# Kernel tuning notes

Hardware: AMD Instinct MI355X
Metric: run time of the kernel (lower is better)

## Reference

```python
import jax, jax.numpy as jnp
import numpy as np

BS, P, D = 64, 300, 1024
NUM_CLASSES = 150


def setup_inputs() -> dict:
    key = jax.random.key(0)
    ks = jax.random.split(key, 12)
    s = 0.02
    return {
        "x": jax.random.normal(ks[0], (BS * P, D), jnp.float32),
        "subject": jax.random.normal(ks[1], (BS, D), jnp.float32),
        "obj": jax.random.normal(ks[2], (BS, D), jnp.float32),
        "relation": jax.random.normal(ks[3], (BS, D), jnp.float32),
        "W_theta": jax.random.normal(ks[4], (D, D), jnp.float32) * s,
        "b_theta": jax.random.normal(ks[5], (D,), jnp.float32) * s,
        "W_pair": jax.random.normal(ks[6], (3 * D, 1), jnp.float32) * s,
        "b_pair": jax.random.normal(ks[7], (1,), jnp.float32) * s,
        "W_cls": jax.random.normal(ks[8], (2 * D, 1), jnp.float32) * s,
        "b_cls": jax.random.normal(ks[9], (1,), jnp.float32) * s,
        "W_bbox": jax.random.normal(ks[10], (D, (NUM_CLASSES + 1) * 4), jnp.float32) * s,
        "b_bbox": jax.random.normal(ks[11], ((NUM_CLASSES + 1) * 4,), jnp.float32) * s,
    }


def reference(x, subject, obj, relation, W_theta, b_theta, W_pair, b_pair,
              W_cls, b_cls, W_bbox, b_bbox):
    bs = relation.shape[0]
    rel = relation @ W_theta + b_theta  # (bs, D)
    xb = x.reshape(bs, P, D)

    # cls_score_pair(concat([x1, x2, rel])) decomposed into 3 sliced matmuls.
    # x1[b,i,j] = x[b,j] (cols), x2[b,i,j] = x[b,i] (rows).
    Wa, Wb, Wc = W_pair[:D, 0], W_pair[D:2 * D, 0], W_pair[2 * D:, 0]
    col_term = xb @ Wa          # (bs, P) -> broadcast over rows i
    row_term = xb @ Wb          # (bs, P) -> broadcast over cols j
    rel_term = rel @ Wc + b_pair[0]  # (bs,)
    pair_score = jax.nn.sigmoid(row_term[:, :, None] + col_term[None if False else slice(None), None, :]
                                + rel_term[:, None, None])  # (bs, P, P)

    # cls_score on [x, subject] and [x, object]
    W1, W2 = W_cls[:D, 0], W_cls[D:, 0]
    xw = xb @ W1                                  # (bs, P)
    s_score = jax.nn.sigmoid(xw + (subject @ W2 + b_cls[0])[:, None])  # (bs, P)
    o_score = jax.nn.sigmoid(xw + (obj @ W2 + b_cls[0])[:, None])      # (bs, P)

    pair_score = pair_score * o_score[:, None, :] * s_score[:, :, None]

    x_subj = jnp.stack([1.0 - s_score, s_score], axis=-1).reshape(-1, 2)
    x_obj = jnp.stack([1.0 - o_score, o_score], axis=-1).reshape(-1, 2)

    bbox_deltas = x @ W_bbox + b_bbox  # (bs*P, (C+1)*4)
    return (x_subj, x_obj, pair_score, bbox_deltas)
```

## Files before the change

### kernel.cpp

```cpp
#include <hip/hip_runtime.h>

#define PP    300
#define DD    1024
#define NOUT  604
#define NROWS 19200
#define OFF_PAIR  76800
#define OFF_BBOX  5836800

typedef unsigned short u16;
typedef __attribute__((ext_vector_type(8))) short bf16x8;
typedef __attribute__((ext_vector_type(4))) float f32x4;

#define GLOBAL_AS __attribute__((address_space(1)))
#define LDS_AS    __attribute__((address_space(3)))

__device__ inline u16 f2bf(float f) {
    unsigned u = __float_as_uint(f);
    return (u16)((u + 0x7fffu + ((u >> 16) & 1u)) >> 16);
}
__device__ inline float dot4(float4 a, float4 b) {
    return fmaf(a.x, b.x, fmaf(a.y, b.y, fmaf(a.z, b.z, a.w * b.w)));
}
__device__ inline float sigmoidf(float z) { return 1.f / (1.f + __expf(-z)); }

__global__ __launch_bounds__(256) void k_rows_raw(
        const float* __restrict__ x, const float* __restrict__ Wpair,
        const float* __restrict__ Wcls,
        float* __restrict__ colv, float* __restrict__ rowp,
        float* __restrict__ cwv, u16* __restrict__ xb,
        const float* __restrict__ Wbbox, u16* __restrict__ Bt,
        const float* __restrict__ Wt, float* __restrict__ v) {
    __shared__ float tile[32][33];
    if (blockIdx.x >= 5440) {
        int wave = threadIdx.x >> 6, lane = threadIdx.x & 63;
        int k = (blockIdx.x - 5440) * 4 + wave;
        const float4* row = (const float4*)(Wt + (size_t)k * DD);
        const float4* wc  = (const float4*)(Wpair + 2 * DD);
        float s = 0.f;
#pragma unroll
        for (int i = 0; i < 4; ++i) s += dot4(row[i * 64 + lane], wc[i * 64 + lane]);
#pragma unroll
        for (int off = 32; off; off >>= 1) s += __shfl_down(s, off, 64);
        if (lane == 0) v[k] = s;
        return;
    }
    if (blockIdx.x >= 4800) {
        int blk = blockIdx.x - 4800;
        int tid = threadIdx.x;
        int k0 = (blk & 31) * 32;
        int n0 = (blk >> 5) * 32;
        int tx = tid & 31;
        int ty = tid >> 5;
#pragma unroll
        for (int i = 0; i < 4; ++i) {
            int k = k0 + ty + i * 8;
            int n = n0 + tx;
            tile[ty + i * 8][tx] = (n < NOUT) ? Wbbox[(size_t)k * NOUT + n] : 0.f;
        }
        __syncthreads();
#pragma unroll
        for (int i = 0; i < 4; ++i) {
            int n = n0 + ty + i * 8;
            int k = k0 + tx;
            Bt[(size_t)n * DD + k] = f2bf(tile[tx][ty + i * 8]);
        }
        return;
    }
    int wave = threadIdx.x >> 6, lane = threadIdx.x & 63;
    int r = blockIdx.x * 4 + wave;
    const float4* xr = (const float4*)(x + (size_t)r * DD);
    const float4* wa = (const float4*)(Wpair);
    const float4* wb = (const float4*)(Wpair + DD);
    const float4* w1 = (const float4*)(Wcls);
    float ca = 0.f, cb = 0.f, cw = 0.f;
#pragma unroll
    for (int i = 0; i < 4; ++i) {
        int idx = i * 64 + lane;
        float4 xv = xr[idx];
        ca += dot4(xv, wa[idx]);
        cb += dot4(xv, wb[idx]);
        cw += dot4(xv, w1[idx]);
        unsigned lo = __builtin_amdgcn_perm(__float_as_uint(xv.y), __float_as_uint(xv.x), 0x07060302u);
        unsigned hi = __builtin_amdgcn_perm(__float_as_uint(xv.w), __float_as_uint(xv.z), 0x07060302u);
        *(uint2*)(xb + (size_t)r * DD + idx * 4) = make_uint2(lo, hi);
    }
#pragma unroll
    for (int off = 32; off; off >>= 1) {
        ca += __shfl_down(ca, off, 64);
        cb += __shfl_down(cb, off, 64);
        cw += __shfl_down(cw, off, 64);
    }
    if (lane == 0) {
        colv[r] = ca;
        rowp[r] = cb;
        cwv[r]  = cw;
    }
}

__global__ void k_scalars(const float* __restrict__ relation, const float* __restrict__ subject,
                          const float* __restrict__ obj, const float* __restrict__ btheta,
                          const float* __restrict__ Wpair, const float* __restrict__ bpair,
                          const float* __restrict__ Wcls, const float* __restrict__ bcls,
                          const float* __restrict__ v,
                          float* __restrict__ relt, float* __restrict__ subc,
                          float* __restrict__ objc) {
    __shared__ float red[4];
    int wave = threadIdx.x >> 6, lane = threadIdx.x & 63;
    int b = blockIdx.x;
    const float4* aa;
    const float4* bb;
    if (wave == 0)      { aa = (const float4*)(relation + (size_t)b * DD); bb = (const float4*)v; }
    else if (wave == 1) { aa = (const float4*)(subject + (size_t)b * DD);  bb = (const float4*)(Wcls + DD); }
    else if (wave == 2) { aa = (const float4*)(obj + (size_t)b * DD);      bb = (const float4*)(Wcls + DD); }
    else                { aa = (const float4*)btheta;                      bb = (const float4*)(Wpair + 2 * DD); }
    float s = 0.f;
#pragma unroll
    for (int i = 0; i < 4; ++i) s += dot4(aa[i * 64 + lane], bb[i * 64 + lane]);
#pragma unroll
    for (int off = 32; off; off >>= 1) s += __shfl_down(s, off, 64);
    if (lane == 0) red[wave] = s;
    __syncthreads();
    if (threadIdx.x == 0) {
        relt[b] = red[0] + red[3] + bpair[0];
        subc[b] = red[1] + bcls[0];
        objc[b] = red[2] + bcls[0];
    }
}

#define BKK 64
#define NSTEP 16

#define WAITCNT_VM(N) asm volatile("s_waitcnt vmcnt(" #N ")" ::: "memory")

#define STAGE_TILE(buf, k0)                                                                  \
    _Pragma("unroll")                                                                        \
    for (int q = 0; q < 4; ++q) {                                                            \
        int rowblk = q * 32 + wave * 8;                                                      \
        const u16* ga = a_base + (size_t)(rowblk + s_row) * DD + (k0) + s_c16 * 8;           \
        __builtin_amdgcn_global_load_lds((const GLOBAL_AS unsigned int*)ga,                  \
                                         (LDS_AS unsigned int*)(As[buf] + rowblk * BKK),     \
                                         16, 0, 0);                                          \
        const u16* gb = b_base + (size_t)(rowblk + s_row) * DD + (k0) + s_c16 * 8;           \
        __builtin_amdgcn_global_load_lds((const GLOBAL_AS unsigned int*)gb,                  \
                                         (LDS_AS unsigned int*)(Bs[buf] + rowblk * BKK),     \
                                         16, 0, 0);                                          \
    }

#define COMPUTE_TILE(buf)                                                                    \
    _Pragma("unroll")                                                                        \
    for (int kk = 0; kk < BKK; kk += 32) {                                                   \
        bf16x8 af[4], bfv[4];                                                                \
        int cx = (((kk >> 3) + quad) ^ (l16 & 7)) * 8;                                       \
        _Pragma("unroll")                                                                    \
        for (int f = 0; f < 4; ++f) {                                                        \
            int m = wr * 64 + f * 16 + l16;                                                  \
            af[f] = *(const bf16x8*)(As[buf] + m * BKK + cx);                                \
            int n = wc * 64 + f * 16 + l16;                                                  \
            bfv[f] = *(const bf16x8*)(Bs[buf] + n * BKK + cx);                               \
        }                                                                                    \
        _Pragma("unroll")                                                                    \
        for (int fi = 0; fi < 4; ++fi)                                                       \
            _Pragma("unroll")                                                                \
            for (int fj = 0; fj < 4; ++fj)                                                   \
                acc[fi][fj] = __builtin_amdgcn_mfma_f32_16x16x32_bf16(                       \
                    af[fi], bfv[fj], acc[fi][fj], 0, 0, 0);                                  \
    }

__global__ __launch_bounds__(256) void k_fused(
        const u16* __restrict__ xb, const u16* __restrict__ bt,
        const float* __restrict__ bias, float* __restrict__ outb,
        const float* __restrict__ rowp, const float* __restrict__ colv,
        const float* __restrict__ cwv,
        const float* __restrict__ relt, const float* __restrict__ subc,
        const float* __restrict__ objc,
        float* __restrict__ outx, float* __restrict__ pout) {
    __shared__ u16 As[2][128 * BKK] __attribute__((aligned(16)));
    __shared__ u16 Bs[2][128 * BKK] __attribute__((aligned(16)));

    int gbid = blockIdx.x;
    if (gbid < 760) {
        int xcd = gbid & 7;
        int rest = gbid >> 3;
        int n_t = rest % 5;
        int m_t = (rest / 5) * 8 + xcd;
        if (m_t >= 150) return;

        int tid = threadIdx.x;
        int wave = tid >> 6;
        int lane = tid & 63;
        int wr = wave >> 1, wc = wave & 1;
        int quad = lane >> 4;
        int l16 = lane & 15;

        f32x4 acc[4][4] = {};

        const u16* a_base = xb + (size_t)m_t * 128 * DD;
        const u16* b_base = bt + (size_t)n_t * 128 * DD;
        int s_row = lane >> 3;
        int s_c16 = (lane & 7) ^ s_row;

        STAGE_TILE(0, 0)

#pragma unroll 1
        for (int t = 0; t < NSTEP; t += 2) {
            STAGE_TILE(1, (t + 1) * BKK)
            WAITCNT_VM(8);
            __builtin_amdgcn_s_barrier();
            COMPUTE_TILE(0)
            __builtin_amdgcn_s_barrier();
            if (t + 2 < NSTEP) {
                STAGE_TILE(0, (t + 2) * BKK)
                WAITCNT_VM(8);
            } else {
                WAITCNT_VM(0);
            }
            __builtin_amdgcn_s_barrier();
            COMPUTE_TILE(1)
            __builtin_amdgcn_s_barrier();
        }

#pragma unroll
        for (int fj = 0; fj < 4; ++fj) {
            int col = n_t * 128 + wc * 64 + fj * 16 + l16;
            if (col < NOUT) {
                float bia = bias[col];
#pragma unroll
                for (int fi = 0; fi < 4; ++fi) {
#pragma unroll
                    for (int rg = 0; rg < 4; ++rg) {
                        int row = m_t * 128 + wr * 64 + fi * 16 + quad * 4 + rg;
                        outb[(size_t)row * NOUT + col] = acc[fi][fj][rg] + bia;
                    }
                }
            }
        }
    } else {
        float* cb_s = (float*)As;
        float* ob_s = ((float*)As) + 300;
        float* cw_s = ((float*)As) + 600;
        int blk = gbid - 760;
        int b = blk / 30;
        int chunk = blk - b * 30;
        int r0 = b * 300 + chunk * 10;
        int tid = threadIdx.x;
        float relt_b = relt[b], subc_b = subc[b], objc_b = objc[b];
        for (int j = tid; j < 300; j += 256) {
            cb_s[j] = colv[b * 300 + j];
            float cwj = cwv[b * 300 + j];
            cw_s[j] = cwj;
            ob_s[j] = sigmoidf(cwj + objc_b);
        }
        __syncthreads();
        if (tid < 150) {
            float c0 = cb_s[2 * tid], c1 = cb_s[2 * tid + 1];
            float o0 = ob_s[2 * tid], o1 = ob_s[2 * tid + 1];
#pragma unroll
            for (int rr = 0; rr < 10; ++rr) {
                int r = r0 + rr;
                int lr = chunk * 10 + rr;
                float rp = rowp[r] + relt_b;
                float ss = sigmoidf(cw_s[lr] + subc_b);
                float p0 = sigmoidf(rp + c0) * o0 * ss;
                float p1 = sigmoidf(rp + c1) * o1 * ss;
                ((float2*)(pout + (size_t)r * 300))[tid] = make_float2(p0, p1);
            }
        } else if (tid < 160) {
            int rr = tid - 150;
            int r = r0 + rr;
            int lr = chunk * 10 + rr;
            float sv = sigmoidf(cw_s[lr] + subc_b);
            float ov = sigmoidf(cw_s[lr] + objc_b);
            ((float2*)outx)[r]         = make_float2(1.f - sv, sv);
            ((float2*)outx)[NROWS + r] = make_float2(1.f - ov, ov);
        }
    }
}

__global__ __launch_bounds__(256) void k_prep(const float* __restrict__ Wbbox, u16* __restrict__ Bt,
                                              const float* __restrict__ Wt, const float* __restrict__ Wpair,
                                              float* __restrict__ v) {
    __shared__ float tile[32][33];
    int blk = blockIdx.x;
    int tid = threadIdx.x;
    if (blk < 640) {
        int k0 = (blk & 31) * 32;
        int n0 = (blk >> 5) * 32;
        int tx = tid & 31;
        int ty = tid >> 5;
#pragma unroll
        for (int i = 0; i < 4; ++i) {
            int k = k0 + ty + i * 8;
            int n = n0 + tx;
            tile[ty + i * 8][tx] = (n < NOUT) ? Wbbox[(size_t)k * NOUT + n] : 0.f;
        }
        __syncthreads();
#pragma unroll
        for (int i = 0; i < 4; ++i) {
            int n = n0 + ty + i * 8;
            int k = k0 + tx;
            Bt[(size_t)n * DD + k] = f2bf(tile[tx][ty + i * 8]);
        }
    } else {
        int wave = tid >> 6, lane = tid & 63;
        int k = (blk - 640) * 4 + wave;
        const float4* row = (const float4*)(Wt + (size_t)k * DD);
        const float4* wc  = (const float4*)(Wpair + 2 * DD);
        float s = 0.f;
#pragma unroll
        for (int i = 0; i < 4; ++i) s += dot4(row[i * 64 + lane], wc[i * 64 + lane]);
#pragma unroll
        for (int off = 32; off; off >>= 1) s += __shfl_down(s, off, 64);
        if (lane == 0) v[k] = s;
    }
}

__global__ __launch_bounds__(256) void k_rows_sa(
        const float* __restrict__ x, const float* __restrict__ Wpair,
        const float* __restrict__ Wcls,
        const float* __restrict__ relt, const float* __restrict__ subc,
        const float* __restrict__ objc,
        float* __restrict__ colv, float* __restrict__ rowp,
        float* __restrict__ sarr, float* __restrict__ oarr,
        float* __restrict__ out) {
    int wave = threadIdx.x >> 6, lane = threadIdx.x & 63;
    int r = blockIdx.x * 4 + wave;
    const float4* xr = (const float4*)(x + (size_t)r * DD);
    const float4* wa = (const float4*)(Wpair);
    const float4* wb = (const float4*)(Wpair + DD);
    const float4* w1 = (const float4*)(Wcls);
    float ca = 0.f, cb = 0.f, cw = 0.f;
#pragma unroll
    for (int i = 0; i < 4; ++i) {
        int idx = i * 64 + lane;
        float4 xv = xr[idx];
        ca += dot4(xv, wa[idx]);
        cb += dot4(xv, wb[idx]);
        cw += dot4(xv, w1[idx]);
    }
#pragma unroll
    for (int off = 32; off; off >>= 1) {
        ca += __shfl_down(ca, off, 64);
        cb += __shfl_down(cb, off, 64);
        cw += __shfl_down(cw, off, 64);
    }
    if (lane == 0) {
        int b = r / 300;
        float s = sigmoidf(cw + subc[b]);
        float o = sigmoidf(cw + objc[b]);
        colv[r] = ca;
        rowp[r] = cb + relt[b];
        sarr[r] = s;
        oarr[r] = o;
        ((float2*)out)[r]         = make_float2(1.f - s, s);
        ((float2*)out)[NROWS + r] = make_float2(1.f - o, o);
    }
}

__global__ __launch_bounds__(192) void k_pair_sa(
        const float* __restrict__ rowp, const float* __restrict__ colv,
        const float* __restrict__ sarr, const float* __restrict__ oarr,
        float* __restrict__ pout) {
    __shared__ float cb_s[300];
    __shared__ float ob_s[300];
    int blk = blockIdx.x;
    int b = blk / 30;
    int chunk = blk - b * 30;
    int r0 = b * 300 + chunk * 10;
    int tid = threadIdx.x;
    for (int j = tid; j < 300; j += 192) {
        cb_s[j] = colv[b * 300 + j];
        ob_s[j] = oarr[b * 300 + j];
    }
    __syncthreads();
    if (tid < 150) {
        float c0 = cb_s[2 * tid], c1 = cb_s[2 * tid + 1];
        float o0 = ob_s[2 * tid], o1 = ob_s[2 * tid + 1];
#pragma unroll
        for (int rr = 0; rr < 10; ++rr) {
            int r = r0 + rr;
            float rp = rowp[r];
            float ss = sarr[r];
            float p0 = sigmoidf(rp + c0) * o0 * ss;
            float p1 = sigmoidf(rp + c1) * o1 * ss;
            ((float2*)(pout + (size_t)r * 300))[tid] = make_float2(p0, p1);
        }
    }
}

__global__ __launch_bounds__(256) void k_gemm(
        const float* __restrict__ x, const u16* __restrict__ bt,
        const float* __restrict__ bias, float* __restrict__ out) {
    __shared__ u16 As[128 * BKK] __attribute__((aligned(16)));
    __shared__ u16 Bs[128 * BKK] __attribute__((aligned(16)));

    int bid = blockIdx.x;
    int xcd = bid & 7;
    int rest = bid >> 3;
    int n_t = rest % 5;
    int m_t = (rest / 5) * 8 + xcd;
    if (m_t >= 150) return;

    int tid = threadIdx.x;
    int wave = tid >> 6;
    int lane = tid & 63;
    int wr = wave >> 1, wc = wave & 1;
    int quad = lane >> 4;
    int l16 = lane & 15;

    f32x4 acc[4][4] = {};

    const float* a_base = x  + (size_t)m_t * 128 * DD;
    const u16*   b_base = bt + (size_t)n_t * 128 * DD;
    int s_row = lane >> 3;
    int s_c16 = lane & 7;
    int arow8 = tid >> 4;
    int acol4 = tid & 15;

    for (int k0 = 0; k0 < DD; k0 += BKK) {
#pragma unroll
        for (int q = 0; q < 4; ++q) {
            int rowblk = q * 32 + wave * 8;
            const u16* gb = b_base + (size_t)(rowblk + s_row) * DD + k0 + s_c16 * 8;
            __builtin_amdgcn_global_load_lds((const GLOBAL_AS unsigned int*)gb,
                                             (LDS_AS unsigned int*)(Bs + rowblk * BKK),
                                             16, 0, 0);
        }
#pragma unroll
        for (int it = 0; it < 8; ++it) {
            int row = it * 16 + arow8;
            float4 av = *(const float4*)(a_base + (size_t)row * DD + k0 + acol4 * 4);
            unsigned lo = __builtin_amdgcn_perm(__float_as_uint(av.y), __float_as_uint(av.x), 0x07060302u);
            unsigned hi = __builtin_amdgcn_perm(__float_as_uint(av.w), __float_as_uint(av.z), 0x07060302u);
            *(uint2*)(As + row * BKK + acol4 * 4) = make_uint2(lo, hi);
        }
        __syncthreads();
#pragma unroll
        for (int kk = 0; kk < BKK; kk += 32) {
            bf16x8 af[4], bfv[4];
#pragma unroll
            for (int f = 0; f < 4; ++f) {
                int m = wr * 64 + f * 16 + l16;
                af[f] = *(const bf16x8*)(As + m * BKK + kk + quad * 8);
                int n = wc * 64 + f * 16 + l16;
                bfv[f] = *(const bf16x8*)(Bs + n * BKK + kk + quad * 8);
            }
#pragma unroll
            for (int fi = 0; fi < 4; ++fi)
#pragma unroll
                for (int fj = 0; fj < 4; ++fj)
                    acc[fi][fj] = __builtin_amdgcn_mfma_f32_16x16x32_bf16(
                        af[fi], bfv[fj], acc[fi][fj], 0, 0, 0);
        }
        __syncthreads();
    }

#pragma unroll
    for (int fj = 0; fj < 4; ++fj) {
        int col = n_t * 128 + wc * 64 + fj * 16 + l16;
        if (col < NOUT) {
            float bia = bias[col];
#pragma unroll
            for (int fi = 0; fi < 4; ++fi) {
#pragma unroll
                for (int rg = 0; rg < 4; ++rg) {
                    int row = m_t * 128 + wr * 64 + fi * 16 + quad * 4 + rg;
                    out[(size_t)row * NOUT + col] = acc[fi][fj][rg] + bia;
                }
            }
        }
    }
}

extern "C" void kernel_launch(void* const* d_in, const int* in_sizes, int n_in,
                              void* d_out, int out_size, void* d_ws, size_t ws_size,
                              hipStream_t stream) {
    const void* P[12] = {};
    int sv[3] = {-1, -1, -1}; int nsv = 0;
    int sc[2] = {-1, -1};     int nsc = 0;
    for (int i = 0; i < n_in; ++i) {
        switch (in_sizes[i]) {
            case 19660800: P[0]  = d_in[i]; break;
            case 65536:    if (nsv < 3) sv[nsv++] = i; break;
            case 1048576:  P[4]  = d_in[i]; break;
            case 1024:     P[5]  = d_in[i]; break;
            case 3072:     P[6]  = d_in[i]; break;
            case 1:        if (nsc < 2) sc[nsc++] = i; break;
            case 2048:     P[8]  = d_in[i]; break;
            case 618496:   P[10] = d_in[i]; break;
            case 604:      P[11] = d_in[i]; break;
            default: break;
        }
    }
    bool alpha = (n_in == 12 && in_sizes[0] == 618496);
    if (alpha) {
        P[2] = d_in[sv[0]]; P[3] = d_in[sv[1]]; P[1] = d_in[sv[2]];
        P[9] = d_in[sc[0]]; P[7] = d_in[sc[1]];
    } else {
        P[1] = d_in[sv[0]]; P[2] = d_in[sv[1]]; P[3] = d_in[sv[2]];
        P[7] = d_in[sc[0]]; P[9] = d_in[sc[1]];
    }
    const float* x        = (const float*)P[0];
    const float* subject  = (const float*)P[1];
    const float* obj      = (const float*)P[2];
    const float* relation = (const float*)P[3];
    const float* W_theta  = (const float*)P[4];
    const float* b_theta  = (const float*)P[5];
    const float* W_pair   = (const float*)P[6];
    const float* b_pair   = (const float*)P[7];
    const float* W_cls    = (const float*)P[8];
    const float* b_cls    = (const float*)P[9];
    const float* W_bbox   = (const float*)P[10];
    const float* b_bbox   = (const float*)P[11];
    float* out = (float*)d_out;

    char* ws = (char*)d_ws;
    float* v    = (float*)(ws + 0);
    float* relt = (float*)(ws + 4096);
    float* subc = (float*)(ws + 4352);
    float* objc = (float*)(ws + 4608);
    float* colv = (float*)(ws + 4864);
    float* rowp = (float*)(ws + 81664);
    float* cwv  = (float*)(ws + 158464);
    float* oarr = (float*)(ws + 235264);
    u16*   Bt   = (u16*)(ws + 312064);
    u16*   Xb   = (u16*)(ws + 1622784);

    const size_t WS_NEED_BF16 = 40944384;
    bool big_ws = (ws_size >= WS_NEED_BF16);

    if (big_ws) {
        k_rows_raw<<<5696, 256, 0, stream>>>(x, W_pair, W_cls, colv, rowp, cwv, Xb,
                                             W_bbox, Bt, W_theta, v);
        k_scalars<<<64, 256, 0, stream>>>(relation, subject, obj, b_theta, W_pair, b_pair,
                                          W_cls, b_cls, v, relt, subc, objc);
        k_fused<<<2680, 256, 0, stream>>>(Xb, Bt, b_bbox, out + OFF_BBOX,
                                          rowp, colv, cwv, relt, subc, objc,
                                          out, out + OFF_PAIR);
    } else {
        k_prep<<<896, 256, 0, stream>>>(W_bbox, Bt, W_theta, W_pair, v);
        k_scalars<<<64, 256, 0, stream>>>(relation, subject, obj, b_theta, W_pair, b_pair,
                                          W_cls, b_cls, v, relt, subc, objc);
        k_rows_sa<<<4800, 256, 0, stream>>>(x, W_pair, W_cls, relt, subc, objc,
                                            colv, rowp, cwv, oarr, out);
        k_pair_sa<<<1920, 192, 0, stream>>>(rowp, colv, cwv, oarr, out + OFF_PAIR);
        k_gemm<<<760, 256, 0, stream>>>(x, Bt, b_bbox, out + OFF_BBOX);
    }
}
```

Before: 202.9 us.

## Fold scalar relation/subject/object kernel into the first prep kernel

Removes the separate k_scalars launch on the big-workspace path. 64 new blocks in the first kernel each compute a full relation@W_theta row, then reduce it against W_pair's third slice, alongside the subject and object dot products. This drops one kernel launch and the dependency on the precomputed v vector. In exchange each of those blocks streams all of W_theta (4 MB, 64 times, mostly from cache), so these blocks could become a long tail.

```diff
diff --git a/kernel.cpp b/kernel.cpp
--- a/kernel.cpp
+++ b/kernel.cpp
@@ -23,25 +23,53 @@
 }
 __device__ inline float sigmoidf(float z) { return 1.f / (1.f + __expf(-z)); }
 
-__global__ __launch_bounds__(256) void k_rows_raw(
+__global__ __launch_bounds__(256) void k_all1(
         const float* __restrict__ x, const float* __restrict__ Wpair,
         const float* __restrict__ Wcls,
         float* __restrict__ colv, float* __restrict__ rowp,
         float* __restrict__ cwv, u16* __restrict__ xb,
         const float* __restrict__ Wbbox, u16* __restrict__ Bt,
-        const float* __restrict__ Wt, float* __restrict__ v) {
+        const float* __restrict__ Wt,
+        const float* __restrict__ relation, const float* __restrict__ subject,
+        const float* __restrict__ obj, const float* __restrict__ btheta,
+        const float* __restrict__ bpair, const float* __restrict__ bcls,
+        float* __restrict__ relt, float* __restrict__ subc, float* __restrict__ objc) {
     __shared__ float tile[32][33];
     if (blockIdx.x >= 5440) {
-        int wave = threadIdx.x >> 6, lane = threadIdx.x & 63;
-        int k = (blockIdx.x - 5440) * 4 + wave;
-        const float4* row = (const float4*)(Wt + (size_t)k * DD);
-        const float4* wc  = (const float4*)(Wpair + 2 * DD);
-        float s = 0.f;
-#pragma unroll
-        for (int i = 0; i < 4; ++i) s += dot4(row[i * 64 + lane], wc[i * 64 + lane]);
-#pragma unroll
-        for (int off = 32; off; off >>= 1) s += __shfl_down(s, off, 64);
-        if (lane == 0) v[k] = s;
+        int b = blockIdx.x - 5440;
+        int tid = threadIdx.x;
+        int wave = tid >> 6, lane = tid & 63;
+        const float* relb = relation + (size_t)b * DD;
+        const float4* wth = (const float4*)Wt;
+        float4 t4 = make_float4(0.f, 0.f, 0.f, 0.f);
+#pragma unroll 4
+        for (int k = 0; k < DD; ++k) {
+            float rk = relb[k];
+            float4 w4 = wth[(size_t)k * 256 + tid];
+            t4.x = fmaf(rk, w4.x, t4.x);
+            t4.y = fmaf(rk, w4.y, t4.y);
+            t4.z = fmaf(rk, w4.z, t4.z);
+            t4.w = fmaf(rk, w4.w, t4.w);
+        }
+        float4 wc4 = ((const float4*)(Wpair + 2 * DD))[tid];
+        float s_rel = dot4(t4, wc4) + dot4(((const float4*)btheta)[tid], wc4);
+        float4 w24 = ((const float4*)(Wcls + DD))[tid];
+        float s_sub = dot4(((const float4*)(subject + (size_t)b * DD))[tid], w24);
+        float s_obj = dot4(((const float4*)(obj + (size_t)b * DD))[tid], w24);
+#pragma unroll
+        for (int off = 32; off; off >>= 1) {
+            s_rel += __shfl_down(s_rel, off, 64);
+            s_sub += __shfl_down(s_sub, off, 64);
+            s_obj += __shfl_down(s_obj, off, 64);
+        }
+        float* red = (float*)tile;
+        if (lane == 0) { red[wave] = s_rel; red[4 + wave] = s_sub; red[8 + wave] = s_obj; }
+        __syncthreads();
+        if (tid == 0) {
+            relt[b] = red[0] + red[1] + red[2] + red[3] + bpair[0];
+            subc[b] = red[4] + red[5] + red[6] + red[7] + bcls[0];
+            objc[b] = red[8] + red[9] + red[10] + red[11] + bcls[0];
+        }
         return;
     }
     if (blockIdx.x >= 4800) {
@@ -94,36 +122,6 @@
         colv[r] = ca;
         rowp[r] = cb;
         cwv[r]  = cw;
-    }
-}
-
-__global__ void k_scalars(const float* __restrict__ relation, const float* __restrict__ subject,
-                          const float* __restrict__ obj, const float* __restrict__ btheta,
-                          const float* __restrict__ Wpair, const float* __restrict__ bpair,
-                          const float* __restrict__ Wcls, const float* __restrict__ bcls,
-                          const float* __restrict__ v,
-                          float* __restrict__ relt, float* __restrict__ subc,
-                          float* __restrict__ objc) {
-    __shared__ float red[4];
-    int wave = threadIdx.x >> 6, lane = threadIdx.x & 63;
-    int b = blockIdx.x;
-    const float4* aa;
-    const float4* bb;
-    if (wave == 0)      { aa = (const float4*)(relation + (size_t)b * DD); bb = (const float4*)v; }
-    else if (wave == 1) { aa = (const float4*)(subject + (size_t)b * DD);  bb = (const float4*)(Wcls + DD); }
-    else if (wave == 2) { aa = (const float4*)(obj + (size_t)b * DD);      bb = (const float4*)(Wcls + DD); }
-    else                { aa = (const float4*)btheta;                      bb = (const float4*)(Wpair + 2 * DD); }
-    float s = 0.f;
-#pragma unroll
-    for (int i = 0; i < 4; ++i) s += dot4(aa[i * 64 + lane], bb[i * 64 + lane]);
-#pragma unroll
-    for (int off = 32; off; off >>= 1) s += __shfl_down(s, off, 64);
-    if (lane == 0) red[wave] = s;
-    __syncthreads();
-    if (threadIdx.x == 0) {
-        relt[b] = red[0] + red[3] + bpair[0];
-        subc[b] = red[1] + bcls[0];
-        objc[b] = red[2] + bcls[0];
     }
 }
 
@@ -314,6 +312,36 @@
     }
 }
 
+__global__ void k_scalars(const float* __restrict__ relation, const float* __restrict__ subject,
+                          const float* __restrict__ obj, const float* __restrict__ btheta,
+                          const float* __restrict__ Wpair, const float* __restrict__ bpair,
+                          const float* __restrict__ Wcls, const float* __restrict__ bcls,
+                          const float* __restrict__ v,
+                          float* __restrict__ relt, float* __restrict__ subc,
+                          float* __restrict__ objc) {
+    __shared__ float red[4];
+    int wave = threadIdx.x >> 6, lane = threadIdx.x & 63;
+    int b = blockIdx.x;
+    const float4* aa;
+    const float4* bb;
+    if (wave == 0)      { aa = (const float4*)(relation + (size_t)b * DD); bb = (const float4*)v; }
+    else if (wave == 1) { aa = (const float4*)(subject + (size_t)b * DD);  bb = (const float4*)(Wcls + DD); }
+    else if (wave == 2) { aa = (const float4*)(obj + (size_t)b * DD);      bb = (const float4*)(Wcls + DD); }
+    else                { aa = (const float4*)btheta;                      bb = (const float4*)(Wpair + 2 * DD); }
+    float s = 0.f;
+#pragma unroll
+    for (int i = 0; i < 4; ++i) s += dot4(aa[i * 64 + lane], bb[i * 64 + lane]);
+#pragma unroll
+    for (int off = 32; off; off >>= 1) s += __shfl_down(s, off, 64);
+    if (lane == 0) red[wave] = s;
+    __syncthreads();
+    if (threadIdx.x == 0) {
+        relt[b] = red[0] + red[3] + bpair[0];
+        subc[b] = red[1] + bcls[0];
+        objc[b] = red[2] + bcls[0];
+    }
+}
+
 __global__ __launch_bounds__(256) void k_rows_sa(
         const float* __restrict__ x, const float* __restrict__ Wpair,
         const float* __restrict__ Wcls,
@@ -529,10 +557,10 @@
     bool big_ws = (ws_size >= WS_NEED_BF16);
 
     if (big_ws) {
-        k_rows_raw<<<5696, 256, 0, stream>>>(x, W_pair, W_cls, colv, rowp, cwv, Xb,
-                                             W_bbox, Bt, W_theta, v);
-        k_scalars<<<64, 256, 0, stream>>>(relation, subject, obj, b_theta, W_pair, b_pair,
-                                          W_cls, b_cls, v, relt, subc, objc);
+        k_all1<<<5504, 256, 0, stream>>>(x, W_pair, W_cls, colv, rowp, cwv, Xb,
+                                         W_bbox, Bt, W_theta,
+                                         relation, subject, obj, b_theta, b_pair, b_cls,
+                                         relt, subc, objc);
         k_fused<<<2680, 256, 0, stream>>>(Xb, Bt, b_bbox, out + OFF_BBOX,
                                           rowp, colv, cwv, relt, subc, objc,
                                           out, out + OFF_PAIR);
```

Result: slower. 328.2 us (+61.8%).
